# Performance work log

Hardware: AMD Instinct MI355X
Metric: run time of the kernel (lower is better)

## Reference

```python
import jax, jax.numpy as jnp
import numpy as np

E, D_IN, D_OUT, T = 8, 2048, 8192, 16384


def setup_inputs() -> dict:
    key = jax.random.key(0)
    k1, k2 = jax.random.split(key, 2)
    inp = jax.random.normal(k1, (T, D_IN), dtype=jnp.float32)
    # kaiming-uniform-ish scale for weight [E, d_out, d_in]
    bound = float(1.0 / np.sqrt(D_IN))
    weight = jax.random.uniform(k2, (E, D_OUT, D_IN), dtype=jnp.float32,
                                minval=-bound, maxval=bound)
    bias = jnp.zeros((E, D_OUT), dtype=jnp.float32)
    # tokens are pre-sorted by expert; equal load here (2048 tokens/expert)
    fwd_expert_count = jnp.full((E,), T // E, dtype=jnp.int32)
    return {"inp": inp, "fwd_expert_count": fwd_expert_count,
            "weight": weight, "bias": bias}


def reference(inp, fwd_expert_count, weight, bias):
    # Grouped GEMM: expert e processes the contiguous slab of
    # fwd_expert_count[e] rows of inp; y = x_e @ W[e].T + b[e].
    counts = np.asarray(fwd_expert_count)          # concrete host ints
    offsets = np.concatenate([[0], np.cumsum(counts)])
    outs = []
    for e in range(counts.shape[0]):
        x_e = inp[offsets[e]:offsets[e + 1]]        # [c_e, d_in]
        outs.append(x_e @ weight[e].T + bias[e])    # [c_e, d_out]
    return jnp.concatenate(outs, axis=0)            # [T, d_out]
```

## Files before the change

### kernel.cpp

```cpp
#include <hip/hip_runtime.h>
#include <stdint.h>

typedef unsigned short u16;
typedef __attribute__((ext_vector_type(8))) short short8;
typedef __attribute__((ext_vector_type(4))) float f32x4;

#define NE   8
#define DIN  2048
#define DOUT 8192
#define NTOK 16384

__device__ __forceinline__ u16 f2bf(float f) {
  uint32_t u = __builtin_bit_cast(uint32_t, f);
  u += 0x7FFFu + ((u >> 16) & 1u);
  return (u16)(u >> 16);
}

__global__ __launch_bounds__(256) void cvt_f32_bf16(const float* __restrict__ src,
                                                    u16* __restrict__ dst, size_t n) {
  size_t i = ((size_t)blockIdx.x * 256 + threadIdx.x) * 8;
  const size_t stride = (size_t)gridDim.x * 256 * 8;
  for (; i < n; i += stride) {
    f32x4 a = *(const f32x4*)(src + i);
    f32x4 b = *(const f32x4*)(src + i + 4);
    short8 o;
    o[0] = (short)f2bf(a[0]); o[1] = (short)f2bf(a[1]);
    o[2] = (short)f2bf(a[2]); o[3] = (short)f2bf(a[3]);
    o[4] = (short)f2bf(b[0]); o[5] = (short)f2bf(b[1]);
    o[6] = (short)f2bf(b[2]); o[7] = (short)f2bf(b[3]);
    *(short8*)(dst + i) = o;
  }
}

#define GLOAD_LDS16(g, l) __builtin_amdgcn_global_load_lds( \
    (const __attribute__((address_space(1))) void*)(g),     \
    (__attribute__((address_space(3))) void*)(l), 16, 0, 0)

__global__ __launch_bounds__(512, 2) void moe_gemm8(
    const u16* __restrict__ Xb, const u16* __restrict__ Wb,
    const int* __restrict__ counts, const float* __restrict__ bias,
    float* __restrict__ C) {
  extern __shared__ u16 sm[];

  const int tid = threadIdx.x;
  const int l = tid & 63;
  const int wid = tid >> 6;
  const int wr = wid >> 2;
  const int wc = wid & 3;

  const int id = blockIdx.x;
  const int swz = (id & 7) * 256 + (id >> 3);
  const int e = swz >> 8;
  const int rem = swz & 255;
  const int tn = rem >> 3;
  const int tm = rem & 7;

  int off = 0;
  for (int i = 0; i < e; ++i) off += counts[i];
  const int row0 = off + tm * 256;
  const int col0 = tn * 256;
  const size_t wbase = (size_t)e * DOUT * DIN + (size_t)col0 * DIN;

  const int rl = l >> 2;
  const int q = (l & 3) ^ ((l >> 3) & 3);
  const int s0 = wid * 2, s1 = s0 + 1;
  const u16* pA0 = Xb + (size_t)(row0 + s0 * 16 + rl) * DIN + q * 8;
  const u16* pA1 = Xb + (size_t)(row0 + s1 * 16 + rl) * DIN + q * 8;
  const u16* pB0 = Wb + wbase + (size_t)(s0 * 16 + rl) * DIN + q * 8;
  const u16* pB1 = Wb + wbase + (size_t)(s1 * 16 + rl) * DIN + q * 8;

  const int f0 = ((l & 15) >> 1) & 3;
  const int gph = (l >> 4) ^ f0;
  const int aoff = (wr * 128 + (l & 15)) * 32 + gph * 8;
  const int boff = (wc * 64 + (l & 15)) * 32 + gph * 8;

  f32x4 acc[8][4] = {};
  short8 a[4], b[4];

#define SMA(buf, kh) (sm + (buf) * 32768 + (kh) * 8192)
#define SMB(buf, kh) (sm + (buf) * 32768 + 16384 + (kh) * 8192)
#define STAGE_A(buf, kt, kh) do { const int ko = (kt) * 64 + (kh) * 32; \
    GLOAD_LDS16(pA0 + ko, SMA(buf, kh) + s0 * 512);                     \
    GLOAD_LDS16(pA1 + ko, SMA(buf, kh) + s1 * 512); } while (0)
#define STAGE_B(buf, kt, kh) do { const int ko = (kt) * 64 + (kh) * 32; \
    GLOAD_LDS16(pB0 + ko, SMB(buf, kh) + s0 * 512);                     \
    GLOAD_LDS16(pB1 + ko, SMB(buf, kh) + s1 * 512); } while (0)
#define RA4(buf, kh, mb) do { _Pragma("unroll") for (int mf = 0; mf < 4; ++mf) \
    a[mf] = *(const short8*)(SMA(buf, kh) + aoff + ((mb) + mf) * 512); } while (0)
#define RB4(buf, kh) do { _Pragma("unroll") for (int nf = 0; nf < 4; ++nf) \
    b[nf] = *(const short8*)(SMB(buf, kh) + boff + nf * 512); } while (0)
#define FENCE() asm volatile("" ::: "memory")
#define BAR() do { FENCE(); __builtin_amdgcn_s_barrier(); FENCE(); } while (0)
#define VMW(N) asm volatile("s_waitcnt vmcnt(" #N ")" ::: "memory")
#define MMQ(mb) do { __builtin_amdgcn_s_setprio(1);                                \
    _Pragma("unroll") for (int mf = 0; mf < 4; ++mf)                               \
      _Pragma("unroll") for (int nf = 0; nf < 4; ++nf)                             \
        acc[(mb) + mf][nf] =                                                       \
          __builtin_amdgcn_mfma_f32_16x16x32_bf16(a[mf], b[nf], acc[(mb) + mf][nf], 0, 0, 0); \
    __builtin_amdgcn_s_setprio(0); } while (0)

  const int NKT = DIN / 64;

  STAGE_A(0, 0, 0); STAGE_B(0, 0, 0); STAGE_A(0, 0, 1); STAGE_B(0, 0, 1);
  VMW(4);
  BAR();

  for (int kt = 0; kt < NKT; kt += 2) {
#define TILE(cur, nxt, t) do {                                          \
    const bool hn = (t) + 1 < NKT;                                      \
                                   \
    RA4(cur, 0, 0); RB4(cur, 0);                                        \
    if (hn) STAGE_A(nxt, (t) + 1, 0);                                   \
    BAR(); MMQ(0);                                                      \
                         \
    RA4(cur, 0, 4);                                                     \
    if (hn) { STAGE_B(nxt, (t) + 1, 0); VMW(4); } else VMW(0);          \
    BAR(); MMQ(4);                                                      \
                                           \
    RA4(cur, 1, 0); RB4(cur, 1);                                        \
    if (hn) STAGE_A(nxt, (t) + 1, 1);                                   \
    BAR(); MMQ(0);                                                      \
                        \
    RA4(cur, 1, 4);                                                     \
    if (hn) { STAGE_B(nxt, (t) + 1, 1); VMW(4); }                       \
    BAR(); MMQ(4); } while (0)
    TILE(0, 1, kt);
    TILE(1, 0, kt + 1);
#undef TILE
  }

  const int rb = row0 + wr * 128 + ((l >> 4) << 2);
  const int cb = col0 + wc * 64 + (l & 15);
#pragma unroll
  for (int n = 0; n < 4; ++n) {
    const int col = cb + n * 16;
    const float bv = bias[e * DOUT + col];
#pragma unroll
    for (int m = 0; m < 8; ++m) {
      const int r = rb + m * 16;
#pragma unroll
      for (int j = 0; j < 4; ++j)
        C[(size_t)(r + j) * DOUT + col] = acc[m][n][j] + bv;
    }
  }
}

__global__ __launch_bounds__(256) void moe_gemm_fused(
    const float* __restrict__ Xf, const float* __restrict__ Wf,
    const int* __restrict__ counts, const float* __restrict__ bias,
    float* __restrict__ C) {
  __shared__ __align__(16) u16 lds[2][2][128 * 32];

  const int tid = threadIdx.x;
  const int lane = tid & 63;
  const int wid = tid >> 6;
  const int wr = wid >> 1;
  const int wc = wid & 1;

  const int id = blockIdx.x;
  const int swz = (id & 7) * ((int)gridDim.x >> 3) + (id >> 3);
  const int e = swz >> 10;
  const int rem = swz & 1023;
  const int tn = rem >> 4;
  const int tml = rem & 15;

  int off = 0;
  for (int i = 0; i < e; ++i) off += counts[i];
  const int row0 = off + tml * 128;
  const int col0 = tn * 128;
  const size_t wbase = (size_t)e * DOUT * DIN + (size_t)col0 * DIN;

  f32x4 acc[4][4] = {};

  auto stage = [&](int buf, int kt) {
#pragma unroll
    for (int s = 0; s < 2; ++s) {
      int i = s * 256 + tid;
      int r = i >> 2, c = i & 3;
      const float* sa = Xf + (size_t)(row0 + r) * DIN + kt * 32 + c * 8;
      const float* sb = Wf + wbase + (size_t)r * DIN + kt * 32 + c * 8;
      f32x4 a0 = *(const f32x4*)sa;
      f32x4 a1 = *(const f32x4*)(sa + 4);
      f32x4 b0 = *(const f32x4*)sb;
      f32x4 b1 = *(const f32x4*)(sb + 4);
      short8 va, vb;
#pragma unroll
      for (int j = 0; j < 4; ++j) {
        va[j] = (short)f2bf(a0[j]); va[j + 4] = (short)f2bf(a1[j]);
        vb[j] = (short)f2bf(b0[j]); vb[j + 4] = (short)f2bf(b1[j]);
      }
      *(short8*)&lds[buf][0][i * 8] = va;
      *(short8*)&lds[buf][1][i * 8] = vb;
    }
  };

  auto compute = [&](int buf) {
    const int kc = lane >> 4;
    const int rr = lane & 15;
    short8 a[4], b[4];
    const u16* lA = lds[buf][0];
    const u16* lB = lds[buf][1];
#pragma unroll
    for (int m = 0; m < 4; ++m)
      a[m] = *(const short8*)(lA + (wr * 64 + m * 16 + rr) * 32 + kc * 8);
#pragma unroll
    for (int n = 0; n < 4; ++n)
      b[n] = *(const short8*)(lB + (wc * 64 + n * 16 + rr) * 32 + kc * 8);
#pragma unroll
    for (int m = 0; m < 4; ++m)
#pragma unroll
      for (int n = 0; n < 4; ++n)
        acc[m][n] = __builtin_amdgcn_mfma_f32_16x16x32_bf16(a[m], b[n], acc[m][n], 0, 0, 0);
  };

  stage(0, 0);
  for (int kt = 0; kt < DIN / 32; ++kt) {
    __syncthreads();
    if (kt + 1 < DIN / 32) stage((kt + 1) & 1, kt + 1);
    compute(kt & 1);
  }

  const int rbase = row0 + wr * 64;
  const int cbase = col0 + wc * 64;
#pragma unroll
  for (int n = 0; n < 4; ++n) {
    const int col = cbase + n * 16 + (lane & 15);
    const float bv = bias[e * DOUT + col];
#pragma unroll
    for (int m = 0; m < 4; ++m) {
      const int r0 = rbase + m * 16 + (lane >> 4) * 4;
#pragma unroll
      for (int j = 0; j < 4; ++j)
        C[(size_t)(r0 + j) * DOUT + col] = acc[m][n][j] + bv;
    }
  }
}

extern "C" void kernel_launch(void* const* d_in, const int* in_sizes, int n_in,
                              void* d_out, int out_size, void* d_ws, size_t ws_size,
                              hipStream_t stream) {
  const float* inp = (const float*)d_in[0];
  const int* counts = (const int*)d_in[1];
  const float* weight = (const float*)d_in[2];
  const float* bias = (const float*)d_in[3];
  float* out = (float*)d_out;

  const size_t nx = (size_t)NTOK * DIN;
  const size_t nw = (size_t)NE * DOUT * DIN;
  const size_t need = (nx + nw) * sizeof(u16);

  if (ws_size >= need) {
    u16* xb = (u16*)d_ws;
    u16* wb = xb + nx;
    cvt_f32_bf16<<<2048, 256, 0, stream>>>(inp, xb, nx);
    cvt_f32_bf16<<<2048, 256, 0, stream>>>(weight, wb, nw);
    const int grid = (NTOK / 256) * (DOUT / 256);
    moe_gemm8<<<grid, 512, 131072, stream>>>(xb, wb, counts, bias, out);
  } else {
    const int grid = (NTOK / 128) * (DOUT / 128);
    moe_gemm_fused<<<grid, 256, 0, stream>>>(inp, weight, counts, bias, out);
  }
}
```

Baseline: 792.2 us.

## Fuse fp32-to-bf16 weight conversion into grouped GEMM B-tile loading

Drops the separate pass that converts the whole weight tensor to bf16. The GEMM now loads fp32 weight tiles into registers, converts them to bf16, and writes them to LDS, staged around the existing double-buffered pipeline with manual vmcnt and lgkmcnt waits. This removes a large extra read and write of the weights through HBM. In exchange, the GEMM reads twice as many bytes per weight tile and spends ALU work on the conversion. It also holds 32 more VGPRs of staging data, which may strain the occupancy target of two 512-thread blocks.

```diff
diff --git a/kernel.cpp b/kernel.cpp
--- a/kernel.cpp
+++ b/kernel.cpp
@@ -37,7 +37,7 @@
     (__attribute__((address_space(3))) void*)(l), 16, 0, 0)
 
 __global__ __launch_bounds__(512, 2) void moe_gemm8(
-    const u16* __restrict__ Xb, const u16* __restrict__ Wb,
+    const u16* __restrict__ Xb, const float* __restrict__ Wf,
     const int* __restrict__ counts, const float* __restrict__ bias,
     float* __restrict__ C) {
   extern __shared__ u16 sm[];
@@ -66,8 +66,8 @@
   const int s0 = wid * 2, s1 = s0 + 1;
   const u16* pA0 = Xb + (size_t)(row0 + s0 * 16 + rl) * DIN + q * 8;
   const u16* pA1 = Xb + (size_t)(row0 + s1 * 16 + rl) * DIN + q * 8;
-  const u16* pB0 = Wb + wbase + (size_t)(s0 * 16 + rl) * DIN + q * 8;
-  const u16* pB1 = Wb + wbase + (size_t)(s1 * 16 + rl) * DIN + q * 8;
+  const float* pBf0 = Wf + wbase + (size_t)(s0 * 16 + rl) * DIN + q * 8;
+  const float* pBf1 = Wf + wbase + (size_t)(s1 * 16 + rl) * DIN + q * 8;
 
   const int f0 = ((l & 15) >> 1) & 3;
   const int gph = (l >> 4) ^ f0;
@@ -76,15 +76,26 @@
 
   f32x4 acc[8][4] = {};
   short8 a[4], b[4];
+  f32x4 bs0[4], bs1[4];
 
 #define SMA(buf, kh) (sm + (buf) * 32768 + (kh) * 8192)
 #define SMB(buf, kh) (sm + (buf) * 32768 + 16384 + (kh) * 8192)
 #define STAGE_A(buf, kt, kh) do { const int ko = (kt) * 64 + (kh) * 32; \
     GLOAD_LDS16(pA0 + ko, SMA(buf, kh) + s0 * 512);                     \
     GLOAD_LDS16(pA1 + ko, SMA(buf, kh) + s1 * 512); } while (0)
-#define STAGE_B(buf, kt, kh) do { const int ko = (kt) * 64 + (kh) * 32; \
-    GLOAD_LDS16(pB0 + ko, SMB(buf, kh) + s0 * 512);                     \
-    GLOAD_LDS16(pB1 + ko, SMB(buf, kh) + s1 * 512); } while (0)
+#define BLD(arr, kt, kh) do { const int ko = (kt) * 64 + (kh) * 32; \
+    arr[0] = *(const f32x4*)(pBf0 + ko);                            \
+    arr[1] = *(const f32x4*)(pBf0 + ko + 4);                        \
+    arr[2] = *(const f32x4*)(pBf1 + ko);                            \
+    arr[3] = *(const f32x4*)(pBf1 + ko + 4); } while (0)
+#define BWR(buf, kh, arr) do {                                           \
+    short8 v0, v1;                                                       \
+    _Pragma("unroll") for (int j = 0; j < 4; ++j) {                      \
+      v0[j] = (short)f2bf(arr[0][j]); v0[4 + j] = (short)f2bf(arr[1][j]);\
+      v1[j] = (short)f2bf(arr[2][j]); v1[4 + j] = (short)f2bf(arr[3][j]);\
+    }                                                                    \
+    *(short8*)(SMB(buf, kh) + (s0 * 16 + rl) * 32 + (l & 3) * 8) = v0;   \
+    *(short8*)(SMB(buf, kh) + (s1 * 16 + rl) * 32 + (l & 3) * 8) = v1; } while (0)
 #define RA4(buf, kh, mb) do { _Pragma("unroll") for (int mf = 0; mf < 4; ++mf) \
     a[mf] = *(const short8*)(SMA(buf, kh) + aoff + ((mb) + mf) * 512); } while (0)
 #define RB4(buf, kh) do { _Pragma("unroll") for (int nf = 0; nf < 4; ++nf) \
@@ -92,6 +103,7 @@
 #define FENCE() asm volatile("" ::: "memory")
 #define BAR() do { FENCE(); __builtin_amdgcn_s_barrier(); FENCE(); } while (0)
 #define VMW(N) asm volatile("s_waitcnt vmcnt(" #N ")" ::: "memory")
+#define LGKM0() asm volatile("s_waitcnt lgkmcnt(0)" ::: "memory")
 #define MMQ(mb) do { __builtin_amdgcn_s_setprio(1);                                \
     _Pragma("unroll") for (int mf = 0; mf < 4; ++mf)                               \
       _Pragma("unroll") for (int nf = 0; nf < 4; ++nf)                             \
@@ -101,28 +113,32 @@
 
   const int NKT = DIN / 64;
 
-  STAGE_A(0, 0, 0); STAGE_B(0, 0, 0); STAGE_A(0, 0, 1); STAGE_B(0, 0, 1);
+  BLD(bs0, 0, 0); BLD(bs1, 0, 1);
+  STAGE_A(0, 0, 0); STAGE_A(0, 0, 1);
   VMW(4);
+  BWR(0, 0, bs0); BWR(0, 1, bs1);
+  VMW(0); LGKM0();
   BAR();
 
   for (int kt = 0; kt < NKT; kt += 2) {
 #define TILE(cur, nxt, t) do {                                          \
     const bool hn = (t) + 1 < NKT;                                      \
-                                   \
+                \
     RA4(cur, 0, 0); RB4(cur, 0);                                        \
-    if (hn) STAGE_A(nxt, (t) + 1, 0);                                   \
+    if (hn) { BLD(bs0, (t) + 1, 0); STAGE_A(nxt, (t) + 1, 0); }         \
     BAR(); MMQ(0);                                                      \
-                         \
+                      \
     RA4(cur, 0, 4);                                                     \
-    if (hn) { STAGE_B(nxt, (t) + 1, 0); VMW(4); } else VMW(0);          \
+    if (hn) { BLD(bs1, (t) + 1, 1); STAGE_A(nxt, (t) + 1, 1);           \
+              VMW(8); BWR(nxt, 0, bs0); }                               \
     BAR(); MMQ(4);                                                      \
-                                           \
+                                    \
     RA4(cur, 1, 0); RB4(cur, 1);                                        \
-    if (hn) STAGE_A(nxt, (t) + 1, 1);                                   \
+    if (hn) { VMW(2); BWR(nxt, 1, bs1); }                               \
     BAR(); MMQ(0);                                                      \
-                        \
+          \
     RA4(cur, 1, 4);                                                     \
-    if (hn) { STAGE_B(nxt, (t) + 1, 1); VMW(4); }                       \
+    if (hn) { VMW(0); LGKM0(); }                                        \
     BAR(); MMQ(4); } while (0)
     TILE(0, 1, kt);
     TILE(1, 0, kt + 1);
@@ -246,16 +262,13 @@
   float* out = (float*)d_out;
 
   const size_t nx = (size_t)NTOK * DIN;
-  const size_t nw = (size_t)NE * DOUT * DIN;
-  const size_t need = (nx + nw) * sizeof(u16);
+  const size_t need = nx * sizeof(u16);
 
   if (ws_size >= need) {
     u16* xb = (u16*)d_ws;
-    u16* wb = xb + nx;
-    cvt_f32_bf16<<<2048, 256, 0, stream>>>(inp, xb, nx);
-    cvt_f32_bf16<<<2048, 256, 0, stream>>>(weight, wb, nw);
+    cvt_f32_bf16<<<1024, 256, 0, stream>>>(inp, xb, nx);
     const int grid = (NTOK / 256) * (DOUT / 256);
-    moe_gemm8<<<grid, 512, 131072, stream>>>(xb, wb, counts, bias, out);
+    moe_gemm8<<<grid, 512, 131072, stream>>>(xb, weight, counts, bias, out);
   } else {
     const int grid = (NTOK / 128) * (DOUT / 128);
     moe_gemm_fused<<<grid, 256, 0, stream>>>(inp, weight, counts, bias, out);
```

Result: slower. 1.276 ms (+61.1%).
